# Kernel tuning notes

Measured on AMD Instinct MI355X. Metric: run time of the kernel, lower is better.

The kernel has to match this reference:

```python
import jax, jax.numpy as jnp
import numpy as np

BLUR = 0.01
SQRT2 = np.sqrt(2.0).astype(np.float32)


def setup_inputs() -> dict:
    key = jax.random.key(0)
    ks = jax.random.split(key, 6)
    B, N, M, DF = 4, 4096, 4096, 16
    src = jax.random.normal(ks[0], (B, N, 3), dtype=jnp.float32)
    tgt = jax.random.normal(ks[1], (B, M, 3), dtype=jnp.float32)
    # small feature scale so C_ij / (2*blur^2) stays in a numerically sane range
    src_fea = jax.random.normal(ks[2], (B, N, DF), dtype=jnp.float32) * 0.01
    tgt_fea = jax.random.normal(ks[3], (B, M, DF), dtype=jnp.float32) * 0.01
    # dual potentials from the (opaque) Sinkhorn solve; O(blur^2) so F/blur^2 ~ O(1)
    F_i = jax.random.normal(ks[4], (B, N), dtype=jnp.float32) * (BLUR ** 2)
    G_j = jax.random.normal(ks[5], (B, M), dtype=jnp.float32) * (BLUR ** 2)
    return {"src": src, "tgt": tgt, "src_fea": src_fea, "tgt_fea": tgt_fea,
            "F_i": F_i, "G_j": G_j}


def _solve_rigid(x, y, w):
    # x: BxNxD points, y: BxNxD mapped points, w: BxNx1 weights
    B, N, D = x.shape
    sum_w = jnp.sum(w, axis=1, keepdims=True)                 # Bx1x1
    mu_x = jnp.sum(x * w, axis=1, keepdims=True) / sum_w      # Bx1xD
    mu_y = jnp.sum(y * w, axis=1, keepdims=True) / sum_w
    wx_hat = (x - mu_x) * w
    wy_hat = (y - mu_y) * w
    a = jnp.einsum('bnd,bne->bde', wy_hat, wx_hat)            # BxDxD = wy^T @ wx
    u, s, vh = jnp.linalg.svd(a)                              # a = u @ diag(s) @ vh
    v = jnp.swapaxes(vh, -1, -2)                              # torch.svd's V
    det = jnp.linalg.det(u @ v)                               # (B,)
    c = jnp.ones((B, D), dtype=x.dtype).at[:, -1].set(det)
    r = (u * c[:, :, None]) @ vh                              # (u*c) @ v^T
    t = mu_y - jnp.swapaxes(r @ jnp.swapaxes(mu_x, 1, 2), 1, 2)
    return r, t.reshape(B, D)


def reference(src, tgt, src_fea, tgt_fea, F_i, G_j):
    # weights are all ones -> log(a_i)=log(b_j)=0, weight1 divide is a no-op
    inv = 1.0 / (SQRT2 * BLUR)
    xx = src_fea * inv                                        # BxNxDf
    yy = tgt_fea * inv                                        # BxMxDf
    f_i = F_i / (BLUR ** 2)                                   # BxN
    g_j = G_j / (BLUR ** 2)                                   # BxM
    # C_ij = ||xx_i - yy_j||^2 via expansion
    x2 = jnp.sum(xx * xx, axis=-1)                            # BxN
    y2 = jnp.sum(yy * yy, axis=-1)                            # BxM
    xy = jnp.einsum('bnd,bmd->bnm', xx, yy)                   # BxNxM
    log_P = (f_i - x2)[:, :, None] + (g_j - y2)[:, None, :] + 2.0 * xy
    lse = jax.nn.logsumexp(log_P, axis=2)                     # BxN
    P_norm = jnp.exp(log_P - lse[:, :, None])                 # softmax over M
    mapped_position = jnp.einsum('bnm,bmd->bnd', P_norm, tgt) # sumsoftmaxweight
    mapped_mass_ratio = jnp.exp(lse)[:, :, None]              # exp(logP).sum(2)/1
    rotation, trans = _solve_rigid(src, mapped_position, mapped_mass_ratio)
    return rotation, trans
```

## Files before the change

kernel.cpp:

```cpp
#include <hip/hip_runtime.h>
#include <hip/hip_bf16.h>
#include <math.h>

#define BB 4
#define NN 4096
#define MM 4096
#define JC 32
#define CHUNK (MM / JC)

#define INVF  70.71067811865475f
#define IB2   10000.0f
#define LOG2E 1.4426950408889634f

#define WS_YY   0
#define WS_TG4  (WS_YY + BB*MM*16)
#define WS_PART (WS_TG4 + BB*MM*4)
#define WS_BLK  (WS_PART + BB*NN*JC*4)

__global__ __launch_bounds__(256) void prep_kernel(
    const float* __restrict__ tgt_fea, const float* __restrict__ G_j,
    const float* __restrict__ tgt, float* __restrict__ ws) {
  int idx = blockIdx.x * 256 + threadIdx.x;
  const float4* tf = (const float4*)tgt_fea + (size_t)idx * 4;
  float4 a[4];
  float y2n = 0.f;
  #pragma unroll
  for (int k = 0; k < 4; ++k) {
    a[k] = tf[k];
    a[k].x *= INVF; a[k].y *= INVF; a[k].z *= INVF; a[k].w *= INVF;
    y2n += a[k].x*a[k].x + a[k].y*a[k].y + a[k].z*a[k].z + a[k].w*a[k].w;
  }
  const float SC = 2.f * LOG2E;
  float4* yy = (float4*)(ws + WS_YY) + (size_t)idx * 4;
  #pragma unroll
  for (int k = 0; k < 4; ++k) {
    float4 s = a[k];
    s.x *= SC; s.y *= SC; s.z *= SC; s.w *= SC;
    yy[k] = s;
  }
  float gyl = LOG2E * (G_j[idx] * IB2 - y2n);
  float4 t4 = make_float4(tgt[idx*3+0], tgt[idx*3+1], tgt[idx*3+2], gyl);
  ((float4*)(ws + WS_TG4))[idx] = t4;
}

__global__ __launch_bounds__(256, 4) void attn_kernel(
    const float* __restrict__ src_fea, const float* __restrict__ ws,
    float* __restrict__ partial) {
  __shared__ float  yyt[CHUNK][16];
  __shared__ float4 tg4s[CHUNK];
  int tid = threadIdx.x;
  int b = blockIdx.z;
  int iA = blockIdx.x * 512 + tid;
  int iB = iA + 256;
  int gA = b * NN + iA, gB = b * NN + iB;

  const float4* sfA = (const float4*)src_fea + (size_t)gA * 4;
  const float4* sfB = (const float4*)src_fea + (size_t)gB * 4;
  float4 qa0 = sfA[0], qa1 = sfA[1], qa2 = sfA[2], qa3 = sfA[3];
  float4 qb0 = sfB[0], qb1 = sfB[1], qb2 = sfB[2], qb3 = sfB[3];
  qa0.x*=INVF; qa0.y*=INVF; qa0.z*=INVF; qa0.w*=INVF;
  qa1.x*=INVF; qa1.y*=INVF; qa1.z*=INVF; qa1.w*=INVF;
  qa2.x*=INVF; qa2.y*=INVF; qa2.z*=INVF; qa2.w*=INVF;
  qa3.x*=INVF; qa3.y*=INVF; qa3.z*=INVF; qa3.w*=INVF;
  qb0.x*=INVF; qb0.y*=INVF; qb0.z*=INVF; qb0.w*=INVF;
  qb1.x*=INVF; qb1.y*=INVF; qb1.z*=INVF; qb1.w*=INVF;
  qb2.x*=INVF; qb2.y*=INVF; qb2.z*=INVF; qb2.w*=INVF;
  qb3.x*=INVF; qb3.y*=INVF; qb3.z*=INVF; qb3.w*=INVF;

  int col0 = b * MM + blockIdx.y * CHUNK;
  {
    const float4* yy = (const float4*)(ws + WS_YY);
    #pragma unroll
    for (int r = 0; r < 2; ++r) {
      int e = tid + r * 256;
      ((float4*)yyt[e >> 2])[e & 3] = yy[(size_t)(col0 + (e >> 2)) * 4 + (e & 3)];
    }
    if (tid < CHUNK)
      tg4s[tid] = ((const float4*)(ws + WS_TG4))[col0 + tid];
  }
  __syncthreads();

  float SA = 0.f, TA0 = 0.f, TA1 = 0.f, TA2 = 0.f;
  float SB = 0.f, TB0 = 0.f, TB1 = 0.f, TB2 = 0.f;

  #pragma unroll 4
  for (int jj = 0; jj < CHUNK; ++jj) {
    const float4* yr = (const float4*)yyt[jj];
    float4 y0 = yr[0], y1 = yr[1], y2 = yr[2], y3 = yr[3];
    float4 tg = tg4s[jj];
    float dA0 = fmaf(qa0.x, y0.x, fmaf(qa0.y, y0.y, fmaf(qa0.z, y0.z, fmaf(qa0.w, y0.w, tg.w))));
    float dA1 = fmaf(qa1.x, y1.x, fmaf(qa1.y, y1.y, fmaf(qa1.z, y1.z, qa1.w * y1.w)));
    float dA2 = fmaf(qa2.x, y2.x, fmaf(qa2.y, y2.y, fmaf(qa2.z, y2.z, qa2.w * y2.w)));
    float dA3 = fmaf(qa3.x, y3.x, fmaf(qa3.y, y3.y, fmaf(qa3.z, y3.z, qa3.w * y3.w)));
    float dB0 = fmaf(qb0.x, y0.x, fmaf(qb0.y, y0.y, fmaf(qb0.z, y0.z, fmaf(qb0.w, y0.w, tg.w))));
    float dB1 = fmaf(qb1.x, y1.x, fmaf(qb1.y, y1.y, fmaf(qb1.z, y1.z, qb1.w * y1.w)));
    float dB2 = fmaf(qb2.x, y2.x, fmaf(qb2.y, y2.y, fmaf(qb2.z, y2.z, qb2.w * y2.w)));
    float dB3 = fmaf(qb3.x, y3.x, fmaf(qb3.y, y3.y, fmaf(qb3.z, y3.z, qb3.w * y3.w)));
    float pA = __builtin_amdgcn_exp2f((dA0 + dA1) + (dA2 + dA3));
    float pB = __builtin_amdgcn_exp2f((dB0 + dB1) + (dB2 + dB3));
    SA += pA;
    TA0 = fmaf(pA, tg.x, TA0); TA1 = fmaf(pA, tg.y, TA1); TA2 = fmaf(pA, tg.z, TA2);
    SB += pB;
    TB0 = fmaf(pB, tg.x, TB0); TB1 = fmaf(pB, tg.y, TB1); TB2 = fmaf(pB, tg.z, TB2);
  }
  ((float4*)partial)[(size_t)gA * JC + blockIdx.y] = make_float4(SA, TA0, TA1, TA2);
  ((float4*)partial)[(size_t)gB * JC + blockIdx.y] = make_float4(SB, TB0, TB1, TB2);
}

__global__ __launch_bounds__(256) void combine_kernel(
    const float* __restrict__ partial, const float* __restrict__ src_fea,
    const float* __restrict__ src, const float* __restrict__ F_i,
    double* __restrict__ blockpart) {
  int b = blockIdx.x, xb = blockIdx.y, tid = threadIdx.x;
  int i = xb * 256 + tid;
  int g = b * NN + i;

  const float4* pr = (const float4*)partial + (size_t)g * JC;
  float S = 0.f, T0 = 0.f, T1 = 0.f, T2 = 0.f;
  #pragma unroll
  for (int c = 0; c < JC; ++c) {
    float4 v = pr[c];
    S += v.x; T0 += v.y; T1 += v.z; T2 += v.w;
  }
  float invS = 1.f / S;
  float y0 = T0 * invS, y1 = T1 * invS, y2 = T2 * invS;

  const float4* sfp = (const float4*)src_fea + (size_t)g * 4;
  float4 a0 = sfp[0], a1 = sfp[1], a2 = sfp[2], a3 = sfp[3];
  a0.x*=INVF; a0.y*=INVF; a0.z*=INVF; a0.w*=INVF;
  a1.x*=INVF; a1.y*=INVF; a1.z*=INVF; a1.w*=INVF;
  a2.x*=INVF; a2.y*=INVF; a2.z*=INVF; a2.w*=INVF;
  a3.x*=INVF; a3.y*=INVF; a3.z*=INVF; a3.w*=INVF;
  float x2 = a0.x*a0.x + a0.y*a0.y + a0.z*a0.z + a0.w*a0.w
           + a1.x*a1.x + a1.y*a1.y + a1.z*a1.z + a1.w*a1.w
           + a2.x*a2.x + a2.y*a2.y + a2.z*a2.z + a2.w*a2.w
           + a3.x*a3.x + a3.y*a3.y + a3.z*a3.z + a3.w*a3.w;
  float w = __builtin_amdgcn_exp2f((F_i[g] * IB2 - x2) * LOG2E
                                   + __builtin_amdgcn_logf(S));

  float px = src[(size_t)g * 3 + 0];
  float py = src[(size_t)g * 3 + 1];
  float pz = src[(size_t)g * 3 + 2];

  double acc[23];
  double wd = (double)w, w2 = wd * wd;
  acc[0]  = wd;
  acc[1]  = wd * px;  acc[2]  = wd * py;  acc[3]  = wd * pz;
  acc[4]  = wd * y0;  acc[5]  = wd * y1;  acc[6]  = wd * y2;
  acc[7]  = w2;
  acc[8]  = w2 * px;  acc[9]  = w2 * py;  acc[10] = w2 * pz;
  acc[11] = w2 * y0;  acc[12] = w2 * y1;  acc[13] = w2 * y2;
  acc[14] = w2 * y0 * px; acc[15] = w2 * y0 * py; acc[16] = w2 * y0 * pz;
  acc[17] = w2 * y1 * px; acc[18] = w2 * y1 * py; acc[19] = w2 * y1 * pz;
  acc[20] = w2 * y2 * px; acc[21] = w2 * y2 * py; acc[22] = w2 * y2 * pz;

  #pragma unroll
  for (int k = 0; k < 23; ++k) {
    #pragma unroll
    for (int off = 32; off > 0; off >>= 1)
      acc[k] += __shfl_down(acc[k], off, 64);
  }
  __shared__ double red[4][23];
  int wave = tid >> 6, lane = tid & 63;
  if (lane == 0) {
    #pragma unroll
    for (int k = 0; k < 23; ++k) red[wave][k] = acc[k];
  }
  __syncthreads();
  if (tid < 23) {
    double s = red[0][tid] + red[1][tid] + red[2][tid] + red[3][tid];
    blockpart[((size_t)b * 16 + xb) * 23 + tid] = s;
  }
}

__device__ __forceinline__ double det3(const double M[3][3]) {
  return M[0][0] * (M[1][1] * M[2][2] - M[1][2] * M[2][1])
       - M[0][1] * (M[1][0] * M[2][2] - M[1][2] * M[2][0])
       + M[0][2] * (M[1][0] * M[2][1] - M[1][1] * M[2][0]);
}

__global__ void finalize_kernel(const double* __restrict__ blockpart,
                                float* __restrict__ out) {
  int b = threadIdx.x;
  if (b >= BB) return;
  double mo[23];
  #pragma unroll
  for (int k = 0; k < 23; ++k) mo[k] = 0.0;
  for (int xb = 0; xb < 16; ++xb)
    #pragma unroll
    for (int k = 0; k < 23; ++k) mo[k] += blockpart[((size_t)b * 16 + xb) * 23 + k];

  double sw = mo[0];
  double mux[3] = { mo[1] / sw, mo[2] / sw, mo[3] / sw };
  double muy[3] = { mo[4] / sw, mo[5] / sw, mo[6] / sw };
  double sw2 = mo[7];
  double A[3][3];
  for (int d = 0; d < 3; ++d)
    for (int e = 0; e < 3; ++e)
      A[d][e] = mo[14 + d * 3 + e] - muy[d] * mo[8 + e] - mux[e] * mo[11 + d]
              + sw2 * muy[d] * mux[e];

  double ATA[3][3];
  for (int p = 0; p < 3; ++p)
    for (int q = 0; q < 3; ++q)
      ATA[p][q] = A[0][p] * A[0][q] + A[1][p] * A[1][q] + A[2][p] * A[2][q];

  double V[3][3] = { {1,0,0}, {0,1,0}, {0,0,1} };
  for (int sweep = 0; sweep < 12; ++sweep) {
    for (int pair = 0; pair < 3; ++pair) {
      int p = (pair == 2) ? 1 : 0;
      int q = (pair == 0) ? 1 : 2;
      double apq = ATA[p][q];
      if (fabs(apq) < 1e-300) continue;
      double tau = (ATA[q][q] - ATA[p][p]) / (2.0 * apq);
      double tt = ((tau >= 0.0) ? 1.0 : -1.0) / (fabs(tau) + sqrt(1.0 + tau * tau));
      double c = 1.0 / sqrt(1.0 + tt * tt), sn = tt * c;
      for (int k = 0; k < 3; ++k) {
        double akp = ATA[k][p], akq = ATA[k][q];
        ATA[k][p] = c * akp - sn * akq;
        ATA[k][q] = sn * akp + c * akq;
      }
      for (int k = 0; k < 3; ++k) {
        double apk = ATA[p][k], aqk = ATA[q][k];
        ATA[p][k] = c * apk - sn * aqk;
        ATA[q][k] = sn * apk + c * aqk;
      }
      for (int k = 0; k < 3; ++k) {
        double vkp = V[k][p], vkq = V[k][q];
        V[k][p] = c * vkp - sn * vkq;
        V[k][q] = sn * vkp + c * vkq;
      }
    }
  }

  double U[3][3];
  for (int k = 0; k < 3; ++k) {
    double sv = sqrt(fmax(ATA[k][k], 0.0));
    double u0 = A[0][0] * V[0][k] + A[0][1] * V[1][k] + A[0][2] * V[2][k];
    double u1 = A[1][0] * V[0][k] + A[1][1] * V[1][k] + A[1][2] * V[2][k];
    double u2 = A[2][0] * V[0][k] + A[2][1] * V[1][k] + A[2][2] * V[2][k];
    double inv = (sv > 1e-300) ? 1.0 / sv : 0.0;
    U[0][k] = u0 * inv; U[1][k] = u1 * inv; U[2][k] = u2 * inv;
  }

  double dd = det3(U) * det3(V);
  double R[3][3];
  for (int d = 0; d < 3; ++d)
    for (int e = 0; e < 3; ++e)
      R[d][e] = U[d][0] * V[e][0] + U[d][1] * V[e][1] + U[d][2] * V[e][2];
  R[2][0] *= dd; R[2][1] *= dd; R[2][2] *= dd;

  double tr[3];
  for (int d = 0; d < 3; ++d)
    tr[d] = muy[d] - (R[d][0] * mux[0] + R[d][1] * mux[1] + R[d][2] * mux[2]);

  for (int d = 0; d < 3; ++d)
    for (int e = 0; e < 3; ++e)
      out[b * 9 + d * 3 + e] = (float)R[d][e];
  out[BB * 9 + b * 3 + 0] = (float)tr[0];
  out[BB * 9 + b * 3 + 1] = (float)tr[1];
  out[BB * 9 + b * 3 + 2] = (float)tr[2];
}

extern "C" void kernel_launch(void* const* d_in, const int* in_sizes, int n_in,
                              void* d_out, int out_size, void* d_ws, size_t ws_size,
                              hipStream_t stream) {
  const float* src     = (const float*)d_in[0];
  const float* tgt     = (const float*)d_in[1];
  const float* src_fea = (const float*)d_in[2];
  const float* tgt_fea = (const float*)d_in[3];
  const float* F_i     = (const float*)d_in[4];
  const float* G_j     = (const float*)d_in[5];
  float* ws  = (float*)d_ws;
  float* out = (float*)d_out;
  double* blockpart = (double*)(ws + WS_BLK);

  prep_kernel<<<BB * MM / 256, 256, 0, stream>>>(tgt_fea, G_j, tgt, ws);
  dim3 grid(NN / 512, JC, BB);
  attn_kernel<<<grid, 256, 0, stream>>>(src_fea, ws, ws + WS_PART);
  dim3 cgrid(BB, 16);
  combine_kernel<<<cgrid, 256, 0, stream>>>(ws + WS_PART, src_fea, src, F_i, blockpart);
  finalize_kernel<<<1, 64, 0, stream>>>(blockpart, out);
}
```

Baseline: 138.3 us.

## Fuse target prep into attention kernel, raise row register blocking, transpose partials

Removes the separate prep kernel: each attention block now loads and scales its own target-feature chunk, computing y2 and g terms through lane shuffles. Each thread now handles four source rows instead of two, which raises reuse of each shared-memory target row. The number of column chunks doubles, and the partial buffer is laid out chunk-major so the combine kernel's reads are coalesced. The finalize kernel parallelises its moment sum over threads and drops from 12 to 8 Jacobi sweeps, which risks slightly lower SVD precision. The extra register pressure from 64 query floats per thread may lower occupancy, and target prep work is now repeated across source blocks.

```diff
diff --git a/kernel.cpp b/kernel.cpp
--- a/kernel.cpp
+++ b/kernel.cpp
@@ -5,106 +5,94 @@
 #define BB 4
 #define NN 4096
 #define MM 4096
-#define JC 32
+#define JC 64
 #define CHUNK (MM / JC)
+#define RR 4
 
 #define INVF  70.71067811865475f
 #define IB2   10000.0f
+#define INV2  5000.0f
 #define LOG2E 1.4426950408889634f
-
-#define WS_YY   0
-#define WS_TG4  (WS_YY + BB*MM*16)
-#define WS_PART (WS_TG4 + BB*MM*4)
-#define WS_BLK  (WS_PART + BB*NN*JC*4)
-
-__global__ __launch_bounds__(256) void prep_kernel(
-    const float* __restrict__ tgt_fea, const float* __restrict__ G_j,
-    const float* __restrict__ tgt, float* __restrict__ ws) {
-  int idx = blockIdx.x * 256 + threadIdx.x;
-  const float4* tf = (const float4*)tgt_fea + (size_t)idx * 4;
-  float4 a[4];
-  float y2n = 0.f;
-  #pragma unroll
-  for (int k = 0; k < 4; ++k) {
-    a[k] = tf[k];
-    a[k].x *= INVF; a[k].y *= INVF; a[k].z *= INVF; a[k].w *= INVF;
-    y2n += a[k].x*a[k].x + a[k].y*a[k].y + a[k].z*a[k].z + a[k].w*a[k].w;
-  }
-  const float SC = 2.f * LOG2E;
-  float4* yy = (float4*)(ws + WS_YY) + (size_t)idx * 4;
-  #pragma unroll
-  for (int k = 0; k < 4; ++k) {
-    float4 s = a[k];
-    s.x *= SC; s.y *= SC; s.z *= SC; s.w *= SC;
-    yy[k] = s;
-  }
-  float gyl = LOG2E * (G_j[idx] * IB2 - y2n);
-  float4 t4 = make_float4(tgt[idx*3+0], tgt[idx*3+1], tgt[idx*3+2], gyl);
-  ((float4*)(ws + WS_TG4))[idx] = t4;
-}
+#define SCY   (INVF * 2.0f * LOG2E)
+
+#define PART_F 0
+#define BLK_F  (BB * JC * NN * 4)
 
 __global__ __launch_bounds__(256, 4) void attn_kernel(
-    const float* __restrict__ src_fea, const float* __restrict__ ws,
+    const float* __restrict__ src_fea, const float* __restrict__ tgt_fea,
+    const float* __restrict__ G_j, const float* __restrict__ tgt,
     float* __restrict__ partial) {
   __shared__ float  yyt[CHUNK][16];
   __shared__ float4 tg4s[CHUNK];
   int tid = threadIdx.x;
-  int b = blockIdx.z;
-  int iA = blockIdx.x * 512 + tid;
-  int iB = iA + 256;
-  int gA = b * NN + iA, gB = b * NN + iB;
-
-  const float4* sfA = (const float4*)src_fea + (size_t)gA * 4;
-  const float4* sfB = (const float4*)src_fea + (size_t)gB * 4;
-  float4 qa0 = sfA[0], qa1 = sfA[1], qa2 = sfA[2], qa3 = sfA[3];
-  float4 qb0 = sfB[0], qb1 = sfB[1], qb2 = sfB[2], qb3 = sfB[3];
-  qa0.x*=INVF; qa0.y*=INVF; qa0.z*=INVF; qa0.w*=INVF;
-  qa1.x*=INVF; qa1.y*=INVF; qa1.z*=INVF; qa1.w*=INVF;
-  qa2.x*=INVF; qa2.y*=INVF; qa2.z*=INVF; qa2.w*=INVF;
-  qa3.x*=INVF; qa3.y*=INVF; qa3.z*=INVF; qa3.w*=INVF;
-  qb0.x*=INVF; qb0.y*=INVF; qb0.z*=INVF; qb0.w*=INVF;
-  qb1.x*=INVF; qb1.y*=INVF; qb1.z*=INVF; qb1.w*=INVF;
-  qb2.x*=INVF; qb2.y*=INVF; qb2.z*=INVF; qb2.w*=INVF;
-  qb3.x*=INVF; qb3.y*=INVF; qb3.z*=INVF; qb3.w*=INVF;
-
-  int col0 = b * MM + blockIdx.y * CHUNK;
+  int b = blockIdx.z, jc = blockIdx.y;
+  int j0 = b * MM + jc * CHUNK;
+
   {
-    const float4* yy = (const float4*)(ws + WS_YY);
-    #pragma unroll
-    for (int r = 0; r < 2; ++r) {
-      int e = tid + r * 256;
-      ((float4*)yyt[e >> 2])[e & 3] = yy[(size_t)(col0 + (e >> 2)) * 4 + (e & 3)];
-    }
-    if (tid < CHUNK)
-      tg4s[tid] = ((const float4*)(ws + WS_TG4))[col0 + tid];
-  }
+    int jl = tid >> 2, part = tid & 3;
+    int jg = j0 + jl;
+    float4 v = *((const float4*)(tgt_fea + (size_t)jg * 16) + part);
+    float ss = v.x*v.x + v.y*v.y + v.z*v.z + v.w*v.w;
+    ss += __shfl_xor(ss, 1, 64);
+    ss += __shfl_xor(ss, 2, 64);
+    ((float4*)yyt[jl])[part] =
+        make_float4(v.x * SCY, v.y * SCY, v.z * SCY, v.w * SCY);
+    if (part == 0) {
+      float y2n = ss * INV2;
+      float gyl = LOG2E * (G_j[jg] * IB2 - y2n);
+      tg4s[jl] = make_float4(tgt[(size_t)jg * 3 + 0],
+                             tgt[(size_t)jg * 3 + 1],
+                             tgt[(size_t)jg * 3 + 2], gyl);
+    }
+  }
+
+  int ib = blockIdx.x * (256 * RR) + tid;
+  float q[RR][16];
+  #pragma unroll
+  for (int r = 0; r < RR; ++r) {
+    const float4* sf = (const float4*)(src_fea
+                     + ((size_t)b * NN + ib + 256 * r) * 16);
+    #pragma unroll
+    for (int k = 0; k < 4; ++k) {
+      float4 v = sf[k];
+      q[r][4*k+0] = v.x * INVF; q[r][4*k+1] = v.y * INVF;
+      q[r][4*k+2] = v.z * INVF; q[r][4*k+3] = v.w * INVF;
+    }
+  }
+
   __syncthreads();
 
-  float SA = 0.f, TA0 = 0.f, TA1 = 0.f, TA2 = 0.f;
-  float SB = 0.f, TB0 = 0.f, TB1 = 0.f, TB2 = 0.f;
-
-  #pragma unroll 4
+  float T0[RR], T1[RR], T2[RR], Sr[RR];
+  #pragma unroll
+  for (int r = 0; r < RR; ++r) { T0[r]=0.f; T1[r]=0.f; T2[r]=0.f; Sr[r]=0.f; }
+
+  #pragma unroll 2
   for (int jj = 0; jj < CHUNK; ++jj) {
     const float4* yr = (const float4*)yyt[jj];
     float4 y0 = yr[0], y1 = yr[1], y2 = yr[2], y3 = yr[3];
     float4 tg = tg4s[jj];
-    float dA0 = fmaf(qa0.x, y0.x, fmaf(qa0.y, y0.y, fmaf(qa0.z, y0.z, fmaf(qa0.w, y0.w, tg.w))));
-    float dA1 = fmaf(qa1.x, y1.x, fmaf(qa1.y, y1.y, fmaf(qa1.z, y1.z, qa1.w * y1.w)));
-    float dA2 = fmaf(qa2.x, y2.x, fmaf(qa2.y, y2.y, fmaf(qa2.z, y2.z, qa2.w * y2.w)));
-    float dA3 = fmaf(qa3.x, y3.x, fmaf(qa3.y, y3.y, fmaf(qa3.z, y3.z, qa3.w * y3.w)));
-    float dB0 = fmaf(qb0.x, y0.x, fmaf(qb0.y, y0.y, fmaf(qb0.z, y0.z, fmaf(qb0.w, y0.w, tg.w))));
-    float dB1 = fmaf(qb1.x, y1.x, fmaf(qb1.y, y1.y, fmaf(qb1.z, y1.z, qb1.w * y1.w)));
-    float dB2 = fmaf(qb2.x, y2.x, fmaf(qb2.y, y2.y, fmaf(qb2.z, y2.z, qb2.w * y2.w)));
-    float dB3 = fmaf(qb3.x, y3.x, fmaf(qb3.y, y3.y, fmaf(qb3.z, y3.z, qb3.w * y3.w)));
-    float pA = __builtin_amdgcn_exp2f((dA0 + dA1) + (dA2 + dA3));
-    float pB = __builtin_amdgcn_exp2f((dB0 + dB1) + (dB2 + dB3));
-    SA += pA;
-    TA0 = fmaf(pA, tg.x, TA0); TA1 = fmaf(pA, tg.y, TA1); TA2 = fmaf(pA, tg.z, TA2);
-    SB += pB;
-    TB0 = fmaf(pB, tg.x, TB0); TB1 = fmaf(pB, tg.y, TB1); TB2 = fmaf(pB, tg.z, TB2);
-  }
-  ((float4*)partial)[(size_t)gA * JC + blockIdx.y] = make_float4(SA, TA0, TA1, TA2);
-  ((float4*)partial)[(size_t)gB * JC + blockIdx.y] = make_float4(SB, TB0, TB1, TB2);
+    #pragma unroll
+    for (int r = 0; r < RR; ++r) {
+      float d0 = fmaf(q[r][0],  y0.x, fmaf(q[r][1],  y0.y,
+                 fmaf(q[r][2],  y0.z, fmaf(q[r][3],  y0.w, tg.w))));
+      float d1 = fmaf(q[r][4],  y1.x, fmaf(q[r][5],  y1.y,
+                 fmaf(q[r][6],  y1.z, q[r][7]  * y1.w)));
+      float d2 = fmaf(q[r][8],  y2.x, fmaf(q[r][9],  y2.y,
+                 fmaf(q[r][10], y2.z, q[r][11] * y2.w)));
+      float d3 = fmaf(q[r][12], y3.x, fmaf(q[r][13], y3.y,
+                 fmaf(q[r][14], y3.z, q[r][15] * y3.w)));
+      float p = __builtin_amdgcn_exp2f((d0 + d1) + (d2 + d3));
+      Sr[r] += p;
+      T0[r] = fmaf(p, tg.x, T0[r]);
+      T1[r] = fmaf(p, tg.y, T1[r]);
+      T2[r] = fmaf(p, tg.z, T2[r]);
+    }
+  }
+
+  float4* pp = (float4*)partial + (size_t)(b * JC + jc) * NN;
+  #pragma unroll
+  for (int r = 0; r < RR; ++r)
+    pp[ib + 256 * r] = make_float4(T0[r], T1[r], T2[r], Sr[r]);
 }
 
 __global__ __launch_bounds__(256) void combine_kernel(
@@ -115,26 +103,23 @@
   int i = xb * 256 + tid;
   int g = b * NN + i;
 
-  const float4* pr = (const float4*)partial + (size_t)g * JC;
   float S = 0.f, T0 = 0.f, T1 = 0.f, T2 = 0.f;
-  #pragma unroll
+  #pragma unroll 8
   for (int c = 0; c < JC; ++c) {
-    float4 v = pr[c];
-    S += v.x; T0 += v.y; T1 += v.z; T2 += v.w;
+    float4 v = ((const float4*)partial)[(size_t)(b * JC + c) * NN + i];
+    T0 += v.x; T1 += v.y; T2 += v.z; S += v.w;
   }
   float invS = 1.f / S;
   float y0 = T0 * invS, y1 = T1 * invS, y2 = T2 * invS;
 
   const float4* sfp = (const float4*)src_fea + (size_t)g * 4;
-  float4 a0 = sfp[0], a1 = sfp[1], a2 = sfp[2], a3 = sfp[3];
-  a0.x*=INVF; a0.y*=INVF; a0.z*=INVF; a0.w*=INVF;
-  a1.x*=INVF; a1.y*=INVF; a1.z*=INVF; a1.w*=INVF;
-  a2.x*=INVF; a2.y*=INVF; a2.z*=INVF; a2.w*=INVF;
-  a3.x*=INVF; a3.y*=INVF; a3.z*=INVF; a3.w*=INVF;
-  float x2 = a0.x*a0.x + a0.y*a0.y + a0.z*a0.z + a0.w*a0.w
-           + a1.x*a1.x + a1.y*a1.y + a1.z*a1.z + a1.w*a1.w
-           + a2.x*a2.x + a2.y*a2.y + a2.z*a2.z + a2.w*a2.w
-           + a3.x*a3.x + a3.y*a3.y + a3.z*a3.z + a3.w*a3.w;
+  float ss = 0.f;
+  #pragma unroll
+  for (int k = 0; k < 4; ++k) {
+    float4 a = sfp[k];
+    ss += a.x*a.x + a.y*a.y + a.z*a.z + a.w*a.w;
+  }
+  float x2 = ss * INV2;
   float w = __builtin_amdgcn_exp2f((F_i[g] * IB2 - x2) * LOG2E
                                    + __builtin_amdgcn_logf(S));
 
@@ -181,14 +166,21 @@
 
 __global__ void finalize_kernel(const double* __restrict__ blockpart,
                                 float* __restrict__ out) {
-  int b = threadIdx.x;
-  if (b >= BB) return;
+  __shared__ double sm[BB][23];
+  int tid = threadIdx.x;
+  int b = tid >> 6, lane = tid & 63;
+  if (lane < 23) {
+    double s = 0.0;
+    for (int xb = 0; xb < 16; ++xb)
+      s += blockpart[((size_t)b * 16 + xb) * 23 + lane];
+    sm[b][lane] = s;
+  }
+  __syncthreads();
+  if (lane != 0) return;
+
   double mo[23];
   #pragma unroll
-  for (int k = 0; k < 23; ++k) mo[k] = 0.0;
-  for (int xb = 0; xb < 16; ++xb)
-    #pragma unroll
-    for (int k = 0; k < 23; ++k) mo[k] += blockpart[((size_t)b * 16 + xb) * 23 + k];
+  for (int k = 0; k < 23; ++k) mo[k] = sm[b][k];
 
   double sw = mo[0];
   double mux[3] = { mo[1] / sw, mo[2] / sw, mo[3] / sw };
@@ -206,7 +198,7 @@
       ATA[p][q] = A[0][p] * A[0][q] + A[1][p] * A[1][q] + A[2][p] * A[2][q];
 
   double V[3][3] = { {1,0,0}, {0,1,0}, {0,0,1} };
-  for (int sweep = 0; sweep < 12; ++sweep) {
+  for (int sweep = 0; sweep < 8; ++sweep) {
     for (int pair = 0; pair < 3; ++pair) {
       int p = (pair == 2) ? 1 : 0;
       int q = (pair == 0) ? 1 : 2;
@@ -273,12 +265,11 @@
   const float* G_j     = (const float*)d_in[5];
   float* ws  = (float*)d_ws;
   float* out = (float*)d_out;
-  double* blockpart = (double*)(ws + WS_BLK);
-
-  prep_kernel<<<BB * MM / 256, 256, 0, stream>>>(tgt_fea, G_j, tgt, ws);
-  dim3 grid(NN / 512, JC, BB);
-  attn_kernel<<<grid, 256, 0, stream>>>(src_fea, ws, ws + WS_PART);
-  dim3 cgrid(BB, 16);
-  combine_kernel<<<cgrid, 256, 0, stream>>>(ws + WS_PART, src_fea, src, F_i, blockpart);
-  finalize_kernel<<<1, 64, 0, stream>>>(blockpart, out);
-}
+  double* blockpart = (double*)(ws + BLK_F);
+
+  dim3 grid(NN / (256 * RR), JC, BB);
+  attn_kernel<<<grid, 256, 0, stream>>>(src_fea, tgt_fea, G_j, tgt, ws + PART_F);
+  dim3 cgrid(BB, NN / 256);
+  combine_kernel<<<cgrid, 256, 0, stream>>>(ws + PART_F, src_fea, src, F_i, blockpart);
+  finalize_kernel<<<1, 256, 0, stream>>>(blockpart, out);
+}
```

Measured after the change: 144.1 us. 1.04x slower.
